# Optimization experiments

Measured on AMD Instinct MI355X. Metric: run time of the kernel, lower is better.

## Reference

```python
import jax, jax.numpy as jnp
import numpy as np

N = 50000
E = 800000
IN_DIM = 128
HID = 256
NCLASS = 40
ORDER = 3
LOCAL_NOISE = 0.5


def setup_inputs() -> dict:
    key = jax.random.key(0)
    ks = jax.random.split(key, 8)
    feats = jax.random.normal(ks[0], (N, IN_DIM), dtype=jnp.float32)
    edge_row = jax.random.randint(ks[1], (E,), 0, N, dtype=jnp.int32)
    edge_col = jax.random.randint(ks[2], (E,), 0, N, dtype=jnp.int32)
    edge_vals = jax.random.uniform(ks[3], (E,), dtype=jnp.float32) / 16.0  # ~row-normalized adjacency
    W1 = jax.random.normal(ks[4], (IN_DIM, HID), dtype=jnp.float32) * (1.0 / np.sqrt(IN_DIM))
    b1 = jnp.zeros((HID,), dtype=jnp.float32)
    W2 = jax.random.normal(ks[5], (HID, NCLASS), dtype=jnp.float32) * (1.0 / np.sqrt(HID))
    b2 = jnp.zeros((NCLASS,), dtype=jnp.float32)
    return {"feats": feats, "edge_row": edge_row, "edge_col": edge_col,
            "edge_vals": edge_vals, "W1": W1, "b1": b1, "W2": W2, "b2": b2}


def _spmm(edge_row, edge_col, edge_vals, x):
    # y[r] = sum_e vals[e] * x[col[e]] for edges with row[e]==r
    msgs = edge_vals[:, None] * x[edge_col]  # [E, D]
    return jax.ops.segment_sum(msgs, edge_row, num_segments=N)


def reference(feats, edge_row, edge_col, edge_vals, W1, b1, W2, b2):
    # eval path: drop_node scales by (1 - drop_rate)
    x = feats * (1.0 - LOCAL_NOISE)
    # GRANDConv_NX: K-hop propagation with running-sum average
    y = x
    h = x
    for _ in range(ORDER):
        h = _spmm(edge_row, edge_col, edge_vals, h)
        y = y + h
    feat = y / (ORDER + 1.0)
    # MLP (use_bn=False, dropout inactive at eval)
    h1 = jax.nn.relu(feat @ W1 + b1)
    logits = h1 @ W2 + b2
    # MLP.forward applies log_softmax, outer forward applies it again
    out = jax.nn.log_softmax(jax.nn.log_softmax(logits, axis=-1), axis=-1)
    return out
```

## Files before the change

### kernel.cpp

```cpp
#include <hip/hip_runtime.h>
#include <math.h>

#define N_NODES 50000
#define N_EDGES 800000
#define IN_DIM 128
#define HID 256
#define NCLASS 40

#define SCAN_NBLK 49

#define HBLK 256
#define EPB  3125
#define PK   12500
#define CS_G 4
#define CS_HPG 64

typedef __attribute__((ext_vector_type(8))) short short8;
typedef __attribute__((ext_vector_type(4))) float floatx4;
typedef __attribute__((ext_vector_type(4))) unsigned uintx4;

__device__ inline unsigned bf16pair(float a, float b) {
    unsigned ua = __float_as_uint(a), ub = __float_as_uint(b);
    ua = (ua + 0x7fffu + ((ua >> 16) & 1u)) >> 16;
    ub = (ub + 0x7fffu + ((ub >> 16) & 1u)) >> 16;
    return ua | (ub << 16);
}
__device__ inline unsigned bf16bits(float a) {
    unsigned ua = __float_as_uint(a);
    return (ua + 0x7fffu + ((ua >> 16) & 1u)) >> 16;
}
__device__ inline float bf_lo(unsigned u) { return __uint_as_float(u << 16); }
__device__ inline float bf_hi(unsigned u) { return __uint_as_float(u & 0xffff0000u); }

__global__ void prep_kernel(const float4* __restrict__ f4,
                            uint2* __restrict__ fb16,
                            const float* __restrict__ W1,
                            uint4* __restrict__ W1frag) {
    int i = blockIdx.x * blockDim.x + threadIdx.x;
    float4 v = f4[i];
    fb16[i] = make_uint2(bf16pair(v.x, v.y), bf16pair(v.z, v.w));
    if (i < 4096) {
        int f = i;
        int h = f >> 11, rem = f & 2047;
        int t = rem >> 8, s = (rem >> 6) & 3, l = rem & 63;
        int q = l >> 4, n16 = l & 15;
        int n = h * 128 + t * 16 + n16;
        int kb = s * 32 + q * 8;
        unsigned p[4];
        #pragma unroll
        for (int jj = 0; jj < 4; ++jj) {
            float a = W1[(size_t)(kb + 2 * jj) * HID + n];
            float b = W1[(size_t)(kb + 2 * jj + 1) * HID + n];
            p[jj] = bf16pair(a, b);
        }
        W1frag[f] = make_uint4(p[0], p[1], p[2], p[3]);
    }
}

__global__ __launch_bounds__(1024) void hist_kernel(const int* __restrict__ rows,
                                                    unsigned* __restrict__ hist) {
    __shared__ unsigned h[PK];
    int t = threadIdx.x;
    for (int i = t; i < PK / 4; i += 1024)
        ((uint4*)h)[i] = make_uint4(0u, 0u, 0u, 0u);
    __syncthreads();
    int e0 = blockIdx.x * EPB;
    for (int i = t; i < EPB; i += 1024) {
        int r = rows[e0 + i];
        atomicAdd(&h[r >> 2], 1u << ((r & 3) * 8));
    }
    __syncthreads();
    unsigned* out = hist + (size_t)blockIdx.x * PK;
    for (int i = t; i < PK / 4; i += 1024)
        ((uint4*)out)[i] = ((const uint4*)h)[i];
}

__global__ __launch_bounds__(1024) void colscan_kernel(const unsigned* __restrict__ hist,
                                                       unsigned* __restrict__ base,
                                                       unsigned* __restrict__ goff,
                                                       int* __restrict__ counts,
                                                       int* __restrict__ blockSums) {
    __shared__ unsigned lsum[CS_G][256];
    int tid = threadIdx.x;
    int g = tid >> 8;
    int c = tid & 255;
    int colq = blockIdx.x * 256 + c;
    unsigned run = 0;
    if (colq < PK) {
        #pragma unroll 8
        for (int i = 0; i < CS_HPG; ++i) {
            int b = g * CS_HPG + i;
            unsigned v = hist[(size_t)b * PK + colq];
            base[(size_t)b * PK + colq] = run;
            run += v;
        }
    }
    lsum[g][c] = run;
    __syncthreads();
    unsigned off = 0;
    #pragma unroll
    for (int gg = 0; gg < CS_G; ++gg) {
        unsigned v = lsum[gg][c];
        if (gg < g) off += v;
    }
    unsigned tot = off + run;
    if (colq < PK) {
        goff[(size_t)g * PK + colq] = off;
        if (g == CS_G - 1)
            *(int4*)(counts + 4 * colq) = make_int4((int)(tot & 0xffu), (int)((tot >> 8) & 0xffu),
                                                    (int)((tot >> 16) & 0xffu), (int)(tot >> 24));
    }
    int s = 0;
    if (g == CS_G - 1 && colq < PK)
        s = (int)((tot & 0xffu) + ((tot >> 8) & 0xffu) + ((tot >> 16) & 0xffu) + (tot >> 24));
    #pragma unroll
    for (int o = 32; o >= 1; o >>= 1)
        s += __shfl_xor(s, o);
    __shared__ int wsum[16];
    int lane = tid & 63, wid = tid >> 6;
    if (lane == 0) wsum[wid] = s;
    __syncthreads();
    if (tid == 0) {
        int acc = 0;
        #pragma unroll
        for (int i = 0; i < 16; ++i) acc += wsum[i];
        blockSums[blockIdx.x] = acc;
    }
}

__global__ __launch_bounds__(256) void local_scan_kernel(const int* __restrict__ counts,
                                                         const int* __restrict__ blockSums,
                                                         int* __restrict__ row_start) {
    __shared__ int wsum[4];
    __shared__ int boff;
    int t = threadIdx.x;
    if (t < 64) {
        int x = (t < SCAN_NBLK) ? blockSums[t] : 0;
        #pragma unroll
        for (int off = 1; off < 64; off <<= 1) {
            int y = __shfl_up(x, off);
            if (t >= off) x += y;
        }
        int excl = __shfl_up(x, 1);
        if (t == 0) excl = 0;
        if (t == blockIdx.x) boff = excl;
        if (blockIdx.x == SCAN_NBLK - 1 && t == SCAN_NBLK - 1)
            row_start[N_NODES] = x;
    }
    int base = blockIdx.x * 1024 + t * 4;
    int4 c = make_int4(0, 0, 0, 0);
    if (base < N_NODES) c = *(const int4*)(counts + base);
    int s0 = c.x, s1 = s0 + c.y, s2 = s1 + c.z, s3 = s2 + c.w;
    int tsum = s3;
    int lane = t & 63, wid = t >> 6;
    int x = tsum;
    #pragma unroll
    for (int off = 1; off < 64; off <<= 1) {
        int y = __shfl_up(x, off);
        if (lane >= off) x += y;
    }
    if (lane == 63) wsum[wid] = x;
    __syncthreads();
    int woff = 0;
    for (int i = 0; i < 4; ++i)
        if (i < wid) woff += wsum[i];
    int excl = x - tsum + woff + boff;
    if (base < N_NODES) {
        int4 rs = make_int4(excl, excl + s0, excl + s1, excl + s2);
        *(int4*)(row_start + base) = rs;
    }
}

__global__ __launch_bounds__(1024) void scatter2_kernel(const int* __restrict__ rows,
                                                        const int* __restrict__ cols,
                                                        const float* __restrict__ vals,
                                                        const unsigned* __restrict__ base,
                                                        const unsigned* __restrict__ goff,
                                                        const int* __restrict__ row_start,
                                                        unsigned* __restrict__ csr_cv) {
    __shared__ unsigned cur[PK];
    int t = threadIdx.x;
    const uint4* bb = (const uint4*)(base + (size_t)blockIdx.x * PK);
    const uint4* gg = (const uint4*)(goff + (size_t)(blockIdx.x >> 6) * PK);
    for (int i = t; i < PK / 4; i += 1024) {
        uint4 b = bb[i], o = gg[i];
        ((uint4*)cur)[i] = make_uint4(b.x + o.x, b.y + o.y, b.z + o.z, b.w + o.w);
    }
    __syncthreads();
    int e0 = blockIdx.x * EPB;
    for (int i = t; i < EPB; i += 1024) {
        int e = e0 + i;
        int r = rows[e];
        unsigned sh = (unsigned)(r & 3) * 8u;
        unsigned old = atomicAdd(&cur[r >> 2], 1u << sh);
        int pos = row_start[r] + (int)((old >> sh) & 0xffu);
        csr_cv[pos] = ((unsigned)cols[e] << 16) | bf16bits(vals[e]);
    }
}

template <int MODE>
__global__ void spmm_csr(const int* __restrict__ row_start,
                         const unsigned* __restrict__ csr_cv,
                         const uintx4* __restrict__ Hin4,
                         uintx4* __restrict__ Hout4,
                         const float* __restrict__ feats,
                         const uintx4* __restrict__ h1b4,
                         const uintx4* __restrict__ h2b4) {
    int wave = (blockIdx.x * blockDim.x + threadIdx.x) >> 6;
    int lane = threadIdx.x & 63;
    if (wave >= N_NODES) return;
    int p = lane >> 4;
    int q = lane & 15;
    int start = row_start[wave];
    int end   = row_start[wave + 1];
    float acc[8] = {};
    for (int base = start; base < end; base += 64) {
        int idx = base + lane;
        unsigned u = 0;
        if (idx < end) u = __builtin_nontemporal_load(csr_cv + idx);
        int cnt = min(64, end - base);
        for (int j = 0; j < cnt; j += 16) {
            unsigned uj0 = __shfl(u, j + p);
            unsigned uj1 = __shfl(u, j + 4 + p);
            unsigned uj2 = __shfl(u, j + 8 + p);
            unsigned uj3 = __shfl(u, j + 12 + p);
            int c0 = uj0 >> 16, c1 = uj1 >> 16, c2 = uj2 >> 16, c3 = uj3 >> 16;
            float v0 = __uint_as_float(uj0 << 16);
            float v1 = __uint_as_float(uj1 << 16);
            float v2 = __uint_as_float(uj2 << 16);
            float v3 = __uint_as_float(uj3 << 16);
            uintx4 h0 = Hin4[(size_t)c0 * 16 + q];
            uintx4 h1 = Hin4[(size_t)c1 * 16 + q];
            uintx4 h2 = Hin4[(size_t)c2 * 16 + q];
            uintx4 h3 = Hin4[(size_t)c3 * 16 + q];
            acc[0] += v0 * bf_lo(h0.x); acc[1] += v0 * bf_hi(h0.x);
            acc[2] += v0 * bf_lo(h0.y); acc[3] += v0 * bf_hi(h0.y);
            acc[4] += v0 * bf_lo(h0.z); acc[5] += v0 * bf_hi(h0.z);
            acc[6] += v0 * bf_lo(h0.w); acc[7] += v0 * bf_hi(h0.w);
            acc[0] += v1 * bf_lo(h1.x); acc[1] += v1 * bf_hi(h1.x);
            acc[2] += v1 * bf_lo(h1.y); acc[3] += v1 * bf_hi(h1.y);
            acc[4] += v1 * bf_lo(h1.z); acc[5] += v1 * bf_hi(h1.z);
            acc[6] += v1 * bf_lo(h1.w); acc[7] += v1 * bf_hi(h1.w);
            acc[0] += v2 * bf_lo(h2.x); acc[1] += v2 * bf_hi(h2.x);
            acc[2] += v2 * bf_lo(h2.y); acc[3] += v2 * bf_hi(h2.y);
            acc[4] += v2 * bf_lo(h2.z); acc[5] += v2 * bf_hi(h2.z);
            acc[6] += v2 * bf_lo(h2.w); acc[7] += v2 * bf_hi(h2.w);
            acc[0] += v3 * bf_lo(h3.x); acc[1] += v3 * bf_hi(h3.x);
            acc[2] += v3 * bf_lo(h3.y); acc[3] += v3 * bf_hi(h3.y);
            acc[4] += v3 * bf_lo(h3.z); acc[5] += v3 * bf_hi(h3.z);
            acc[6] += v3 * bf_lo(h3.w); acc[7] += v3 * bf_hi(h3.w);
        }
    }
    #pragma unroll
    for (int i = 0; i < 8; ++i) {
        acc[i] += __shfl_xor(acc[i], 16);
        acc[i] += __shfl_xor(acc[i], 32);
    }
    if (p == 0) {
        size_t o16 = (size_t)wave * 16 + q;
        if (MODE == 1) {
            #pragma unroll
            for (int i = 0; i < 8; ++i) acc[i] *= 0.5f;
        } else if (MODE == 2) {
            size_t of = (size_t)wave * IN_DIM + q * 8;
            floatx4 f0 = __builtin_nontemporal_load((const floatx4*)(feats + of));
            floatx4 f1 = __builtin_nontemporal_load((const floatx4*)(feats + of + 4));
            uintx4 a = __builtin_nontemporal_load(h1b4 + o16);
            uintx4 b = __builtin_nontemporal_load(h2b4 + o16);
            acc[0] += 0.5f * f0.x + bf_lo(a.x) + bf_lo(b.x);
            acc[1] += 0.5f * f0.y + bf_hi(a.x) + bf_hi(b.x);
            acc[2] += 0.5f * f0.z + bf_lo(a.y) + bf_lo(b.y);
            acc[3] += 0.5f * f0.w + bf_hi(a.y) + bf_hi(b.y);
            acc[4] += 0.5f * f1.x + bf_lo(a.z) + bf_lo(b.z);
            acc[5] += 0.5f * f1.y + bf_hi(a.z) + bf_hi(b.z);
            acc[6] += 0.5f * f1.z + bf_lo(a.w) + bf_lo(b.w);
            acc[7] += 0.5f * f1.w + bf_hi(a.w) + bf_hi(b.w);
        }
        uintx4 rv;
        rv.x = bf16pair(acc[0], acc[1]);
        rv.y = bf16pair(acc[2], acc[3]);
        rv.z = bf16pair(acc[4], acc[5]);
        rv.w = bf16pair(acc[6], acc[7]);
        __builtin_nontemporal_store(rv, Hout4 + o16);
    }
}

__global__ void gemm1_mfma(const uint4* __restrict__ yb4,
                           const uint4* __restrict__ W1frag,
                           const float* __restrict__ bias1,
                           float* __restrict__ H1) {
    __shared__ uint4 wlds[2048];
    int tid = threadIdx.x;
    int h = blockIdx.y;
    for (int i = tid; i < 2048; i += 256)
        wlds[i] = W1frag[h * 2048 + i];
    __syncthreads();

    int wave = tid >> 6, lane = tid & 63;
    int q = lane >> 4, c16 = lane & 15;
    int row0 = blockIdx.x * 64 + wave * 16;
    int arow = row0 + c16;

    union { uint4 u; short8 v; } au[4], bu;
    if (arow < N_NODES) {
        #pragma unroll
        for (int s = 0; s < 4; ++s)
            au[s].u = yb4[(size_t)arow * 16 + 4 * s + q];
    } else {
        #pragma unroll
        for (int s = 0; s < 4; ++s)
            au[s].u = make_uint4(0u, 0u, 0u, 0u);
    }

    #pragma unroll
    for (int t = 0; t < 8; ++t) {
        floatx4 acc = {0.f, 0.f, 0.f, 0.f};
        #pragma unroll
        for (int s = 0; s < 4; ++s) {
            bu.u = wlds[(t * 4 + s) * 64 + lane];
            acc = __builtin_amdgcn_mfma_f32_16x16x32_bf16(au[s].v, bu.v, acc, 0, 0, 0);
        }
        int col = h * 128 + t * 16 + c16;
        float bs = bias1[col];
        #pragma unroll
        for (int r = 0; r < 4; ++r) {
            int crow = row0 + q * 4 + r;
            if (crow < N_NODES) {
                float v = 0.25f * acc[r] + bs;
                H1[(size_t)crow * HID + col] = v > 0.f ? v : 0.f;
            }
        }
    }
}

#define G2_BM 128
__global__ void gemm2lsm_kernel(const float* __restrict__ H1,
                                const float* __restrict__ W2,
                                const float* __restrict__ b2,
                                float* __restrict__ Out) {
    __shared__ float As[32][G2_BM + 4];
    __shared__ float Bs[32][44];
    int tid = threadIdx.x;
    int rt = tid >> 3;
    int ct = tid & 7;
    int row0 = blockIdx.x * G2_BM;
    float acc[4][5] = {};
    for (int k0 = 0; k0 < HID; k0 += 32) {
        #pragma unroll
        for (int i = tid; i < 1024; i += 256) {
            int r = i >> 3, u = i & 7;
            int gr = row0 + r;
            float4 v = make_float4(0.f, 0.f, 0.f, 0.f);
            if (gr < N_NODES)
                v = *(const float4*)(H1 + (size_t)gr * HID + k0 + u * 4);
            int kb = u * 4;
            As[kb + 0][r] = v.x;
            As[kb + 1][r] = v.y;
            As[kb + 2][r] = v.z;
            As[kb + 3][r] = v.w;
        }
        for (int i = tid; i < 320; i += 256) {
            int r = i / 10, cg = i % 10;
            float4 w = *(const float4*)(W2 + (size_t)(k0 + r) * NCLASS + cg * 4);
            *(float4*)&Bs[r][cg * 4] = w;
        }
        __syncthreads();
        #pragma unroll
        for (int kk = 0; kk < 32; ++kk) {
            float4 a0 = *(const float4*)&As[kk][rt * 4];
            float a[4] = {a0.x, a0.y, a0.z, a0.w};
            float b[5];
            #pragma unroll
            for (int j = 0; j < 5; ++j) b[j] = Bs[kk][ct * 5 + j];
            #pragma unroll
            for (int i = 0; i < 4; ++i)
                #pragma unroll
                for (int j = 0; j < 5; ++j)
                    acc[i][j] += a[i] * b[j];
        }
        __syncthreads();
    }
    float bb[5];
    #pragma unroll
    for (int j = 0; j < 5; ++j) bb[j] = b2[ct * 5 + j];
    #pragma unroll
    for (int i = 0; i < 4; ++i) {
        int gr = row0 + rt * 4 + i;
        float z[5];
        #pragma unroll
        for (int j = 0; j < 5; ++j) z[j] = acc[i][j] + bb[j];
        float m = z[0];
        #pragma unroll
        for (int j = 1; j < 5; ++j) m = fmaxf(m, z[j]);
        #pragma unroll
        for (int off = 1; off < 8; off <<= 1) m = fmaxf(m, __shfl_xor(m, off));
        float s = 0.f;
        #pragma unroll
        for (int j = 0; j < 5; ++j) s += expf(z[j] - m);
        #pragma unroll
        for (int off = 1; off < 8; off <<= 1) s += __shfl_xor(s, off);
        float l1 = m + logf(s);
        #pragma unroll
        for (int j = 0; j < 5; ++j) z[j] -= l1;
        float m2 = z[0];
        #pragma unroll
        for (int j = 1; j < 5; ++j) m2 = fmaxf(m2, z[j]);
        #pragma unroll
        for (int off = 1; off < 8; off <<= 1) m2 = fmaxf(m2, __shfl_xor(m2, off));
        float s2 = 0.f;
        #pragma unroll
        for (int j = 0; j < 5; ++j) s2 += expf(z[j] - m2);
        #pragma unroll
        for (int off = 1; off < 8; off <<= 1) s2 += __shfl_xor(s2, off);
        float l2 = m2 + logf(s2);
        if (gr < N_NODES) {
            float* dst = Out + (size_t)gr * NCLASS + ct * 5;
            #pragma unroll
            for (int j = 0; j < 5; ++j) dst[j] = z[j] - l2;
        }
    }
}

extern "C" void kernel_launch(void* const* d_in, const int* in_sizes, int n_in,
                              void* d_out, int out_size, void* d_ws, size_t ws_size,
                              hipStream_t stream) {
    const float* feats   = (const float*)d_in[0];
    const int*   e_row   = (const int*)d_in[1];
    const int*   e_col   = (const int*)d_in[2];
    const float* e_vals  = (const float*)d_in[3];
    const float* W1      = (const float*)d_in[4];
    const float* b1      = (const float*)d_in[5];
    const float* W2      = (const float*)d_in[6];
    const float* b2      = (const float*)d_in[7];
    float* out = (float*)d_out;

    float* ws    = (float*)d_ws;
    uint4* ybf4  = (uint4*)ws;
    unsigned* hist = (unsigned*)ws;
    uint4* W1frag = (uint4*)(ws + (size_t)N_NODES * IN_DIM / 2);
    int*   counts = (int*)(ws + 3300000);
    unsigned* goff = (unsigned*)(ws + 3400000);
    uint4* fb16_4 = (uint4*)(ws + (size_t)N_NODES * IN_DIM);
    uint4* h1b4  = (uint4*)(ws + (size_t)N_NODES * IN_DIM * 3 / 2);
    uint4* h2b4  = (uint4*)(ws + (size_t)N_NODES * IN_DIM * 2);
    unsigned* basep = (unsigned*)(ws + (size_t)N_NODES * IN_DIM * 5 / 2);
    float* hid   = ws + (size_t)N_NODES * IN_DIM;

    unsigned* csr_cv = (unsigned*)d_out;
    int*   row_start = (int*)d_out + 2 * N_EDGES;
    int*   blockSums = row_start + N_NODES + 4;

    const int ELEMS4 = N_NODES * IN_DIM / 4;
    prep_kernel<<<ELEMS4 / 256, 256, 0, stream>>>((const float4*)feats, (uint2*)fb16_4,
                                                  W1, W1frag);

    hist_kernel<<<HBLK, 1024, 0, stream>>>(e_row, hist);
    colscan_kernel<<<SCAN_NBLK, 1024, 0, stream>>>(hist, basep, goff, counts, blockSums);
    local_scan_kernel<<<SCAN_NBLK, 256, 0, stream>>>(counts, blockSums, row_start);
    scatter2_kernel<<<HBLK, 1024, 0, stream>>>(e_row, e_col, e_vals, basep, goff,
                                               row_start, csr_cv);

    const int SPMM_BLOCKS = N_NODES / 4;
    spmm_csr<1><<<SPMM_BLOCKS, 256, 0, stream>>>(row_start, csr_cv, (const uintx4*)fb16_4,
                                                 (uintx4*)h1b4, nullptr, nullptr, nullptr);
    spmm_csr<0><<<SPMM_BLOCKS, 256, 0, stream>>>(row_start, csr_cv, (const uintx4*)h1b4,
                                                 (uintx4*)h2b4, nullptr, nullptr, nullptr);
    spmm_csr<2><<<SPMM_BLOCKS, 256, 0, stream>>>(row_start, csr_cv, (const uintx4*)h2b4,
                                                 (uintx4*)ybf4, feats,
                                                 (const uintx4*)h1b4, (const uintx4*)h2b4);

    dim3 g1((N_NODES + 63) / 64, 2);
    gemm1_mfma<<<g1, 256, 0, stream>>>(ybf4, W1frag, b1, hid);

    gemm2lsm_kernel<<<(N_NODES + G2_BM - 1) / G2_BM, 256, 0, stream>>>(hid, W2, b2, out);
}
```

Before: 268.9 us.

## Fuse both MLP GEMMs and log-softmax into one MFMA kernel

Replaces the separate gemm1 kernel (which wrote a 50000x256 fp32 hidden matrix to global memory) and the FP32 SIMT gemm2 + log_softmax kernel with a single fused kernel. The hidden activations stay in LDS as bf16, and the second GEMM uses bf16 MFMA with W2 pre-packed into fragments, padded from 40 to 48 columns, in the prep kernel. This removes a large global write and read of the hidden layer plus a kernel launch. In exchange it adds bf16 rounding of the hidden activations, more LDS per block, and serialized W1 reloads within each block.

Result: faster. 234.6 us (-12.8%).

```diff
diff --git a/kernel.cpp b/kernel.cpp
--- a/kernel.cpp
+++ b/kernel.cpp
@@ -35,7 +35,9 @@
 __global__ void prep_kernel(const float4* __restrict__ f4,
                             uint2* __restrict__ fb16,
                             const float* __restrict__ W1,
-                            uint4* __restrict__ W1frag) {
+                            uint4* __restrict__ W1frag,
+                            const float* __restrict__ W2,
+                            uint4* __restrict__ W2frag) {
     int i = blockIdx.x * blockDim.x + threadIdx.x;
     float4 v = f4[i];
     fb16[i] = make_uint2(bf16pair(v.x, v.y), bf16pair(v.z, v.w));
@@ -54,6 +56,21 @@
             p[jj] = bf16pair(a, b);
         }
         W1frag[f] = make_uint4(p[0], p[1], p[2], p[3]);
+    } else if (i < 4096 + 1536) {
+        int f2 = i - 4096;
+        int nt = f2 >> 9;
+        int rem = f2 & 511;
+        int ks = rem >> 6, l = rem & 63;
+        int col = nt * 16 + (l & 15);
+        int k = ks * 32 + (l >> 4) * 8;
+        unsigned p[4];
+        #pragma unroll
+        for (int jj = 0; jj < 4; ++jj) {
+            float a = (col < NCLASS) ? W2[(size_t)(k + 2 * jj) * NCLASS + col] : 0.f;
+            float b = (col < NCLASS) ? W2[(size_t)(k + 2 * jj + 1) * NCLASS + col] : 0.f;
+            p[jj] = bf16pair(a, b);
+        }
+        W2frag[f2] = make_uint4(p[0], p[1], p[2], p[3]);
     }
 }
 
@@ -285,23 +302,22 @@
     }
 }
 
-__global__ void gemm1_mfma(const uint4* __restrict__ yb4,
-                           const uint4* __restrict__ W1frag,
-                           const float* __restrict__ bias1,
-                           float* __restrict__ H1) {
-    __shared__ uint4 wlds[2048];
+#define H1_STRIDE 264
+__global__ __launch_bounds__(256) void mlp_fused(const uint4* __restrict__ yb4,
+                                                 const uint4* __restrict__ W1frag,
+                                                 const uint4* __restrict__ W2frag,
+                                                 const float* __restrict__ bias1,
+                                                 const float* __restrict__ b2,
+                                                 float* __restrict__ Out) {
+    __shared__ uint4 shA[1536];
+    __shared__ unsigned short h1u[64 * H1_STRIDE];
     int tid = threadIdx.x;
-    int h = blockIdx.y;
-    for (int i = tid; i < 2048; i += 256)
-        wlds[i] = W1frag[h * 2048 + i];
-    __syncthreads();
-
-    int wave = tid >> 6, lane = tid & 63;
+    int w = tid >> 6, lane = tid & 63;
     int q = lane >> 4, c16 = lane & 15;
-    int row0 = blockIdx.x * 64 + wave * 16;
-    int arow = row0 + c16;
-
-    union { uint4 u; short8 v; } au[4], bu;
+    int row0 = blockIdx.x * 64;
+    int arow = row0 + w * 16 + c16;
+
+    union { uint4 u; short8 v; } au[4], bu, af;
     if (arow < N_NODES) {
         #pragma unroll
         for (int s = 0; s < 4; ++s)
@@ -312,111 +328,87 @@
             au[s].u = make_uint4(0u, 0u, 0u, 0u);
     }
 
-    #pragma unroll
-    for (int t = 0; t < 8; ++t) {
-        floatx4 acc = {0.f, 0.f, 0.f, 0.f};
-        #pragma unroll
-        for (int s = 0; s < 4; ++s) {
-            bu.u = wlds[(t * 4 + s) * 64 + lane];
-            acc = __builtin_amdgcn_mfma_f32_16x16x32_bf16(au[s].v, bu.v, acc, 0, 0, 0);
-        }
-        int col = h * 128 + t * 16 + c16;
-        float bs = bias1[col];
-        #pragma unroll
-        for (int r = 0; r < 4; ++r) {
-            int crow = row0 + q * 4 + r;
-            if (crow < N_NODES) {
-                float v = 0.25f * acc[r] + bs;
-                H1[(size_t)crow * HID + col] = v > 0.f ? v : 0.f;
+    for (int h = 0; h < 2; ++h) {
+        for (int tq = 0; tq < 2; ++tq) {
+            __syncthreads();
+            #pragma unroll
+            for (int i = tid; i < 1024; i += 256)
+                shA[i] = W1frag[h * 2048 + tq * 1024 + i];
+            __syncthreads();
+            #pragma unroll
+            for (int t2 = 0; t2 < 4; ++t2) {
+                floatx4 acc = {0.f, 0.f, 0.f, 0.f};
+                #pragma unroll
+                for (int s = 0; s < 4; ++s) {
+                    bu.u = shA[(t2 * 4 + s) * 64 + lane];
+                    acc = __builtin_amdgcn_mfma_f32_16x16x32_bf16(au[s].v, bu.v, acc, 0, 0, 0);
+                }
+                int col = h * 128 + (tq * 4 + t2) * 16 + c16;
+                float bs = bias1[col];
+                #pragma unroll
+                for (int r = 0; r < 4; ++r) {
+                    float v = 0.25f * acc[r] + bs;
+                    v = v > 0.f ? v : 0.f;
+                    h1u[(w * 16 + q * 4 + r) * H1_STRIDE + col] =
+                        (unsigned short)bf16bits(v);
+                }
             }
         }
     }
-}
-
-#define G2_BM 128
-__global__ void gemm2lsm_kernel(const float* __restrict__ H1,
-                                const float* __restrict__ W2,
-                                const float* __restrict__ b2,
-                                float* __restrict__ Out) {
-    __shared__ float As[32][G2_BM + 4];
-    __shared__ float Bs[32][44];
-    int tid = threadIdx.x;
-    int rt = tid >> 3;
-    int ct = tid & 7;
-    int row0 = blockIdx.x * G2_BM;
-    float acc[4][5] = {};
-    for (int k0 = 0; k0 < HID; k0 += 32) {
-        #pragma unroll
-        for (int i = tid; i < 1024; i += 256) {
-            int r = i >> 3, u = i & 7;
-            int gr = row0 + r;
-            float4 v = make_float4(0.f, 0.f, 0.f, 0.f);
-            if (gr < N_NODES)
-                v = *(const float4*)(H1 + (size_t)gr * HID + k0 + u * 4);
-            int kb = u * 4;
-            As[kb + 0][r] = v.x;
-            As[kb + 1][r] = v.y;
-            As[kb + 2][r] = v.z;
-            As[kb + 3][r] = v.w;
-        }
-        for (int i = tid; i < 320; i += 256) {
-            int r = i / 10, cg = i % 10;
-            float4 w = *(const float4*)(W2 + (size_t)(k0 + r) * NCLASS + cg * 4);
-            *(float4*)&Bs[r][cg * 4] = w;
-        }
-        __syncthreads();
-        #pragma unroll
-        for (int kk = 0; kk < 32; ++kk) {
-            float4 a0 = *(const float4*)&As[kk][rt * 4];
-            float a[4] = {a0.x, a0.y, a0.z, a0.w};
-            float b[5];
-            #pragma unroll
-            for (int j = 0; j < 5; ++j) b[j] = Bs[kk][ct * 5 + j];
-            #pragma unroll
-            for (int i = 0; i < 4; ++i)
-                #pragma unroll
-                for (int j = 0; j < 5; ++j)
-                    acc[i][j] += a[i] * b[j];
-        }
-        __syncthreads();
-    }
-    float bb[5];
-    #pragma unroll
-    for (int j = 0; j < 5; ++j) bb[j] = b2[ct * 5 + j];
-    #pragma unroll
-    for (int i = 0; i < 4; ++i) {
-        int gr = row0 + rt * 4 + i;
-        float z[5];
-        #pragma unroll
-        for (int j = 0; j < 5; ++j) z[j] = acc[i][j] + bb[j];
-        float m = z[0];
-        #pragma unroll
-        for (int j = 1; j < 5; ++j) m = fmaxf(m, z[j]);
-        #pragma unroll
-        for (int off = 1; off < 8; off <<= 1) m = fmaxf(m, __shfl_xor(m, off));
-        float s = 0.f;
-        #pragma unroll
-        for (int j = 0; j < 5; ++j) s += expf(z[j] - m);
-        #pragma unroll
-        for (int off = 1; off < 8; off <<= 1) s += __shfl_xor(s, off);
+    __syncthreads();
+    #pragma unroll
+    for (int i = tid; i < 1536; i += 256)
+        shA[i] = W2frag[i];
+    __syncthreads();
+
+    floatx4 acc2[3] = {{0.f,0.f,0.f,0.f},{0.f,0.f,0.f,0.f},{0.f,0.f,0.f,0.f}};
+    const unsigned* h1w = (const unsigned*)h1u;
+    #pragma unroll
+    for (int ks = 0; ks < 8; ++ks) {
+        af.u = *(const uint4*)&h1w[(w * 16 + c16) * (H1_STRIDE / 2) + ks * 16 + q * 4];
+        #pragma unroll
+        for (int nt = 0; nt < 3; ++nt) {
+            bu.u = shA[nt * 512 + ks * 64 + lane];
+            acc2[nt] = __builtin_amdgcn_mfma_f32_16x16x32_bf16(af.v, bu.v, acc2[nt], 0, 0, 0);
+        }
+    }
+
+    float bb[3];
+    #pragma unroll
+    for (int nt = 0; nt < 3; ++nt) {
+        int col = nt * 16 + c16;
+        bb[nt] = (col < NCLASS) ? b2[col] : 0.f;
+    }
+    #pragma unroll
+    for (int r = 0; r < 4; ++r) {
+        int gr = row0 + w * 16 + q * 4 + r;
+        float z[3];
+        #pragma unroll
+        for (int nt = 0; nt < 3; ++nt) z[nt] = acc2[nt][r] + bb[nt];
+        if (c16 >= 8) z[2] = -INFINITY;
+        float m = fmaxf(fmaxf(z[0], z[1]), z[2]);
+        #pragma unroll
+        for (int off = 1; off < 16; off <<= 1) m = fmaxf(m, __shfl_xor(m, off));
+        float s = expf(z[0] - m) + expf(z[1] - m) + ((c16 < 8) ? expf(z[2] - m) : 0.f);
+        #pragma unroll
+        for (int off = 1; off < 16; off <<= 1) s += __shfl_xor(s, off);
         float l1 = m + logf(s);
         #pragma unroll
-        for (int j = 0; j < 5; ++j) z[j] -= l1;
-        float m2 = z[0];
-        #pragma unroll
-        for (int j = 1; j < 5; ++j) m2 = fmaxf(m2, z[j]);
-        #pragma unroll
-        for (int off = 1; off < 8; off <<= 1) m2 = fmaxf(m2, __shfl_xor(m2, off));
-        float s2 = 0.f;
-        #pragma unroll
-        for (int j = 0; j < 5; ++j) s2 += expf(z[j] - m2);
-        #pragma unroll
-        for (int off = 1; off < 8; off <<= 1) s2 += __shfl_xor(s2, off);
+        for (int nt = 0; nt < 3; ++nt) z[nt] -= l1;
+        float m2 = fmaxf(fmaxf(z[0], z[1]), z[2]);
+        #pragma unroll
+        for (int off = 1; off < 16; off <<= 1) m2 = fmaxf(m2, __shfl_xor(m2, off));
+        float s2 = expf(z[0] - m2) + expf(z[1] - m2) + ((c16 < 8) ? expf(z[2] - m2) : 0.f);
+        #pragma unroll
+        for (int off = 1; off < 16; off <<= 1) s2 += __shfl_xor(s2, off);
         float l2 = m2 + logf(s2);
         if (gr < N_NODES) {
-            float* dst = Out + (size_t)gr * NCLASS + ct * 5;
             #pragma unroll
-            for (int j = 0; j < 5; ++j) dst[j] = z[j] - l2;
+            for (int nt = 0; nt < 3; ++nt) {
+                int col = nt * 16 + c16;
+                if (col < NCLASS)
+                    Out[(size_t)gr * NCLASS + col] = z[nt] - l2;
+            }
         }
     }
 }
@@ -438,13 +430,13 @@
     uint4* ybf4  = (uint4*)ws;
     unsigned* hist = (unsigned*)ws;
     uint4* W1frag = (uint4*)(ws + (size_t)N_NODES * IN_DIM / 2);
+    uint4* W2frag = (uint4*)(ws + 3250000);
     int*   counts = (int*)(ws + 3300000);
     unsigned* goff = (unsigned*)(ws + 3400000);
     uint4* fb16_4 = (uint4*)(ws + (size_t)N_NODES * IN_DIM);
     uint4* h1b4  = (uint4*)(ws + (size_t)N_NODES * IN_DIM * 3 / 2);
     uint4* h2b4  = (uint4*)(ws + (size_t)N_NODES * IN_DIM * 2);
     unsigned* basep = (unsigned*)(ws + (size_t)N_NODES * IN_DIM * 5 / 2);
-    float* hid   = ws + (size_t)N_NODES * IN_DIM;
 
     unsigned* csr_cv = (unsigned*)d_out;
     int*   row_start = (int*)d_out + 2 * N_EDGES;
@@ -452,7 +444,7 @@
 
     const int ELEMS4 = N_NODES * IN_DIM / 4;
     prep_kernel<<<ELEMS4 / 256, 256, 0, stream>>>((const float4*)feats, (uint2*)fb16_4,
-                                                  W1, W1frag);
+                                                  W1, W1frag, W2, W2frag);
 
     hist_kernel<<<HBLK, 1024, 0, stream>>>(e_row, hist);
     colscan_kernel<<<SCAN_NBLK, 1024, 0, stream>>>(hist, basep, goff, counts, blockSums);
@@ -469,8 +461,5 @@
                                                  (uintx4*)ybf4, feats,
                                                  (const uintx4*)h1b4, (const uintx4*)h2b4);
 
-    dim3 g1((N_NODES + 63) / 64, 2);
-    gemm1_mfma<<<g1, 256, 0, stream>>>(ybf4, W1frag, b1, hid);
-
-    gemm2lsm_kernel<<<(N_NODES + G2_BM - 1) / G2_BM, 256, 0, stream>>>(hid, W2, b2, out);
-}
+    mlp_fused<<<(N_NODES + 63) / 64, 256, 0, stream>>>(ybf4, W1frag, W2frag, b1, b2, out);
+}
```
